# Kernel tuning notes

Hardware: AMD Instinct MI355X
Metric: run time of the kernel (lower is better)

The kernel has to match this reference:

```python
import jax, jax.numpy as jnp
import numpy as np

B, D, S, E = 256, 5, 30, 768
H1, H2, FF, OUT = 512, 512, 256, 2


def setup_inputs() -> dict:
    key = jax.random.key(0)
    ks = iter(jax.random.split(key, 40))

    def p(shape, scale=0.05):
        return jax.random.normal(next(ks), shape, jnp.float32) * scale

    return {
        "sentence_feats": jax.random.normal(next(ks), (B, D, S, E), jnp.float32),
        "time_feats": jax.random.uniform(next(ks), (B, D, S), jnp.float32),
        "len_tweets": jax.random.randint(next(ks), (B, D), 1, S + 1, jnp.int32),
        # TimeLSTM (lstm1)
        "Wd_w": p((H1, H1)), "Wd_b": p((H1,)),
        "Wall_w": p((4 * H1, H1)), "Wall_b": p((4 * H1,)),
        "Uall_w": p((4 * H1, E)), "Uall_b": p((4 * H1,)),
        # attn1
        "A1_W1_w": p((H1, H1)), "A1_W1_b": p((H1,)),
        "A1_W2_w": p((H1, H1)), "A1_W2_b": p((H1,)),
        "A1_V_w": p((1, H1)), "A1_V_b": p((1,)),
        # nn.LSTM (lstm2), gate order i,f,g,o
        "L2_Wih": p((4 * H2, H1)), "L2_Whh": p((4 * H2, H2)),
        "L2_bih": p((4 * H2,)), "L2_bhh": p((4 * H2,)),
        # attn2
        "A2_W1_w": p((H2, H2)), "A2_W1_b": p((H2,)),
        "A2_W2_w": p((H2, H2)), "A2_W2_b": p((H2,)),
        "A2_V_w": p((1, H2)), "A2_V_b": p((1,)),
        # head
        "lin3_w": p((FF, H2)), "lin3_b": p((FF,)),
        "lin4_w": p((OUT, FF)), "lin4_b": p((OUT,)),
    }


def _time_lstm(x, t, Wd_w, Wd_b, Wall_w, Wall_b, Uall_w, Uall_b):
    # x: (N,S,E), t: (N,S) -> o-gate outputs (N,S,H) (the torch module stacks `o`, not `h`)
    N = x.shape[0]
    H = Wd_w.shape[0]
    ux = jnp.einsum('nse,ge->nsg', x, Uall_w) + Uall_b  # (N,S,4H), hoisted out of recurrence

    def step(carry, inp):
        h, c = carry
        ux_s, t_s = inp
        c_s1 = jnp.tanh(c @ Wd_w.T + Wd_b)
        c_adj = c - c_s1 + c_s1 * t_s[:, None]
        gates = jax.nn.sigmoid(h @ Wall_w.T + Wall_b + ux_s)
        f, i, o, c_tmp = jnp.split(gates, 4, axis=1)  # all sigmoid, incl. c_tmp (as in source)
        c = f * c_adj + i * c_tmp
        h = o * jnp.tanh(c)
        return (h, c), o

    init = (jnp.zeros((N, H), x.dtype), jnp.zeros((N, H), x.dtype))
    _, os = jax.lax.scan(step, init, (ux.transpose(1, 0, 2), t.T))
    return os.transpose(1, 0, 2)  # (N,S,H)


def _std_lstm(x, Wih, Whh, bih, bhh):
    # PyTorch nn.LSTM, 1 layer, batch_first. x: (B,T,I) -> (hs (B,T,H), h_n (B,H))
    Bn = x.shape[0]
    H = Whh.shape[1]
    xi = jnp.einsum('bti,gi->btg', x, Wih) + bih + bhh  # (B,T,4H)

    def step(carry, xi_t):
        h, c = carry
        g = xi_t + h @ Whh.T
        i, f, gg, o = jnp.split(g, 4, axis=1)
        c = jax.nn.sigmoid(f) * c + jax.nn.sigmoid(i) * jnp.tanh(gg)
        h = jax.nn.sigmoid(o) * jnp.tanh(c)
        return (h, c), h

    init = (jnp.zeros((Bn, H), x.dtype), jnp.zeros((Bn, H), x.dtype))
    (h_n, _), hs = jax.lax.scan(step, init, xi.transpose(1, 0, 2))
    return hs.transpose(1, 0, 2), h_n


def _forward(sentence_feats, time_feats, Wd_w, Wd_b, Wall_w, Wall_b, Uall_w, Uall_b,
             A1_W1_w, A1_W1_b, A1_W2_w, A1_W2_b, A1_V_w, A1_V_b,
             L2_Wih, L2_Whh, L2_bih, L2_bhh,
             A2_W1_w, A2_W1_b, A2_W2_w, A2_W2_b, A2_V_w, A2_V_b,
             lin3_w, lin3_b, lin4_w, lin4_b, len_tweets):
    x = sentence_feats.transpose(1, 0, 2, 3)  # (D,B,S,E)
    t = time_feats.transpose(1, 0, 2)         # (D,B,S)
    lens = len_tweets.transpose(1, 0)          # (D,B)
    d, b, s, e = x.shape

    # run TimeLSTM over all days at once (days are independent, shared zero init)
    outs = _time_lstm(x.reshape(d * b, s, e), t.reshape(d * b, s),
                      Wd_w, Wd_b, Wall_w, Wall_b, Uall_w, Uall_b).reshape(d, b, s, H1)

    # Faithful to the source's inner loop: temp_hn ends up as the LAST batch
    # element's output at index len-1, shared across the whole batch of that day.
    idx = lens[:, -1] - 1  # (D,)
    last = jnp.take_along_axis(outs[:, -1], idx[:, None, None], axis=1)[:, 0]  # (D,H1)

    # attn1: score = V(tanh(W1(last) + W2(full))), mask by lens, softmax over S
    s1 = jnp.tanh((last @ A1_W1_w.T + A1_W1_b)[:, None, None, :]
                  + jnp.einsum('dbsh,gh->dbsg', outs, A1_W2_w) + A1_W2_b)
    score = jnp.einsum('dbsh,oh->dbso', s1, A1_V_w) + A1_V_b  # (D,B,S,1)
    mask = jnp.arange(s)[None, None, :] < lens[:, :, None]     # (D,B,S)
    score = jnp.where(mask[..., None], score, -jnp.inf)
    aw = jax.nn.softmax(score, axis=2)
    lstm1_out = jnp.sum(aw * outs, axis=2).transpose(1, 0, 2)  # (B,D,H1)

    lstm2_out, hn2 = _std_lstm(lstm1_out, L2_Wih, L2_Whh, L2_bih, L2_bhh)  # (B,D,H2),(B,H2)

    # attn2 over days
    s2 = jnp.tanh((hn2 @ A2_W1_w.T + A2_W1_b)[:, None, :]
                  + lstm2_out @ A2_W2_w.T + A2_W2_b)
    score2 = s2 @ A2_V_w.T + A2_V_b                 # (B,D,1)
    aw2 = jax.nn.softmax(score2, axis=1)
    ctx = jnp.sum(aw2 * lstm2_out, axis=1)          # (B,H2)

    h3 = jax.nn.relu(ctx @ lin3_w.T + lin3_b)       # dropout = identity (eval mode)
    return h3 @ lin4_w.T + lin4_b                   # (B,OUT)


def reference(sentence_feats, time_feats, len_tweets, Wd_w, Wd_b, Wall_w, Wall_b, Uall_w, Uall_b,
              A1_W1_w, A1_W1_b, A1_W2_w, A1_W2_b, A1_V_w, A1_V_b,
              L2_Wih, L2_Whh, L2_bih, L2_bhh,
              A2_W1_w, A2_W1_b, A2_W2_w, A2_W2_b, A2_V_w, A2_V_b,
              lin3_w, lin3_b, lin4_w, lin4_b):
    return _forward(sentence_feats, time_feats, Wd_w, Wd_b, Wall_w, Wall_b, Uall_w, Uall_b,
                    A1_W1_w, A1_W1_b, A1_W2_w, A1_W2_b, A1_V_w, A1_V_b,
                    L2_Wih, L2_Whh, L2_bih, L2_bhh,
                    A2_W1_w, A2_W1_b, A2_W2_w, A2_W2_b, A2_V_w, A2_V_b,
                    lin3_w, lin3_b, lin4_w, lin4_b, len_tweets)
```

## Files before the change

### kernel.cpp

```cpp
#include <hip/hip_runtime.h>
#include <math.h>

typedef _Float16 f16;
typedef _Float16 f16x4 __attribute__((ext_vector_type(4)));
typedef _Float16 f16x8 __attribute__((ext_vector_type(8)));
typedef float f32x4 __attribute__((ext_vector_type(4)));

#define DEV static __device__ __forceinline__

#define OFF_X16    ((size_t)0)
#define OFF_UX     ((size_t)58982400)
#define OFF_OUTS   ((size_t)216268800)
#define OFF_WD     ((size_t)255590400)
#define OFF_WALLP  ((size_t)256114688)
#define OFF_UP     ((size_t)258211840)
#define OFF_W2     ((size_t)261357568)
#define OFF_WIHP   ((size_t)261881856)
#define OFF_WHHP   ((size_t)263979008)
#define OFF_A2W1C  ((size_t)266076160)
#define OFF_A2W2C  ((size_t)266600448)
#define OFF_L3WC   ((size_t)267124736)
#define OFF_BALLP  ((size_t)267386880)
#define OFF_BIHP   ((size_t)267395072)
#define OFF_H16    ((size_t)267403264)
#define OFF_C16    ((size_t)270024704)
#define OFF_C32    ((size_t)272646144)
#define WS_NEED    ((size_t)277889024)
#define OFF_SCORE  ((size_t)0)
#define OFF_W1L    ((size_t)153600)
#define OFF_L1O32  ((size_t)163840)
#define OFF_L1O16  ((size_t)2785280)
#define OFF_XI2    ((size_t)4096000)
#define OFF_C2     ((size_t)14581760)
#define OFF_H2     ((size_t)15630336)
#define OFF_L2O32  ((size_t)16154624)
#define OFF_L2O16  ((size_t)18776064)
#define OFF_U2     ((size_t)20086784)
#define OFF_V2     ((size_t)22708224)
#define OFF_CTX16  ((size_t)23232512)
#define OFF_H3     ((size_t)23494656)

DEV float sigf(float x) { return 1.f / (1.f + __expf(-x)); }
DEV float tanhfast(float x) { float e = __expf(2.f * x); return 1.f - 2.f / (e + 1.f); }
DEV int permrow(int c) { return (((c >> 4) & 3) << 9) | ((c >> 6) << 4) | (c & 15); }

DEV void gload16(const f16* g, f16x8* lds) {
  __builtin_amdgcn_global_load_lds((const __attribute__((address_space(1))) void*)g,
                                   (__attribute__((address_space(3))) void*)lds, 16, 0, 0);
}

DEV void gemm_core(const f16* __restrict__ A, const f16* __restrict__ Bt, int K,
                   int rowBase, int colBase, f16x8* sh, f32x4 (&acc)[4][4]) {
  const int t = threadIdx.x, lane = t & 63, w = t >> 6;
  const int wr = (w >> 1) * 64, wc = (w & 1) * 64;
  const f16* Arow = A + (size_t)rowBase * K;
  const f16* Brow = Bt + (size_t)colBase * K;
  auto stage = [&](f16x8* dstBase, const f16* src, int k0) {
#pragma unroll
    for (int i = 0; i < 4; ++i) {
      int c = i * 256 + t; int r = c >> 3; int cc = (c & 7) ^ (r & 7);
      gload16(src + (size_t)r * K + (k0 + cc * 8), dstBase + i * 256 + (t & 192));
    }
  };
  stage(sh, Arow, 0);
  stage(sh + 2048, Brow, 0);
  const int nk = K >> 6;
  for (int kt = 0; kt < nk; ++kt) {
    const int cur = kt & 1;
    if (kt + 1 < nk) {
      stage(sh + (cur ^ 1) * 1024, Arow, (kt + 1) * 64);
      stage(sh + 2048 + (cur ^ 1) * 1024, Brow, (kt + 1) * 64);
      asm volatile("s_waitcnt vmcnt(8)" ::: "memory");
    } else {
      asm volatile("s_waitcnt vmcnt(0)" ::: "memory");
    }
    __builtin_amdgcn_s_barrier();
    __builtin_amdgcn_sched_barrier(0);
    const f16x8* shA = sh + cur * 1024;
    const f16x8* shB = sh + 2048 + cur * 1024;
    const int rr = lane & 15, chb = lane >> 4;
#pragma unroll
    for (int kk = 0; kk < 2; ++kk) {
      const int ch = kk * 4 + chb;
      f16x8 af[4], bf[4];
#pragma unroll
      for (int m = 0; m < 4; ++m) { int row = wr + m * 16 + rr; af[m] = shA[row * 8 + (ch ^ (row & 7))]; }
#pragma unroll
      for (int n = 0; n < 4; ++n) { int row = wc + n * 16 + rr; bf[n] = shB[row * 8 + (ch ^ (row & 7))]; }
#pragma unroll
      for (int m = 0; m < 4; ++m)
#pragma unroll
        for (int n = 0; n < 4; ++n)
          acc[m][n] = __builtin_amdgcn_mfma_f32_16x16x32_f16(af[m], bf[n], acc[m][n], 0, 0, 0);
    }
    __builtin_amdgcn_sched_barrier(0);
    __builtin_amdgcn_s_barrier();
  }
}

template <int ACT, bool O32, bool O16>
__global__ __launch_bounds__(256, 2) void k_gemm(const f16* __restrict__ A, const f16* __restrict__ Bt,
                                                 int K, int N, const float* __restrict__ bias,
                                                 float* __restrict__ C32, f16* __restrict__ C16) {
  __shared__ f16x8 sh[4096];
  const int rb = blockIdx.y * 128, cb = blockIdx.x * 128;
  f32x4 acc[4][4] = {};
  gemm_core(A, Bt, K, rb, cb, sh, acc);
  const int t = threadIdx.x, lane = t & 63, w = t >> 6;
  const int wr = (w >> 1) * 64, wc = (w & 1) * 64, ec = lane & 15, er = (lane >> 4) * 4;
#pragma unroll
  for (int m = 0; m < 4; ++m)
#pragma unroll
    for (int n = 0; n < 4; ++n) {
      const int c = cb + wc + n * 16 + ec;
      const float bv = bias ? bias[c] : 0.f;
#pragma unroll
      for (int j = 0; j < 4; ++j) {
        const int r = rb + wr + m * 16 + er + j;
        float v = acc[m][n][j] + bv;
        if (ACT == 3) v = fmaxf(v, 0.f);
        if (O32) C32[(size_t)r * N + c] = v;
        if (O16) C16[(size_t)r * N + c] = (f16)v;
      }
    }
}

__global__ __launch_bounds__(256, 1) void k_stepf(
    const f16* __restrict__ hin, const f16* __restrict__ cin16, const float* __restrict__ cin32,
    const f16* __restrict__ Wallp, const f16* __restrict__ Wd16,
    const f16* __restrict__ ux, const float* __restrict__ ballp, const float* __restrict__ Wd_b,
    const float* __restrict__ tf,
    float* __restrict__ cout32, f16* __restrict__ cout16, f16* __restrict__ hout,
    f16* __restrict__ outs, int s) {
  __shared__ f16x8 shA[2048];
  __shared__ f16x8 shB[2048];
  __shared__ f16x8 shC[2048];
  __shared__ f16x8 shD[512];
  const int t = threadIdx.x, lane = t & 63, w = t >> 6;
  const int rb = (blockIdx.x >> 4) * 128;
  const int cg = blockIdx.x & 15;
  const int wr = (w >> 1) * 64, wc = (w & 1) * 64;
  const int rr = lane & 15, chb = lane >> 4;
  f32x4 acc[4][4] = {};
  f32x4 acc2[4] = {};
  const f16* Ah = hin + (size_t)rb * 512;
  const f16* Bw = Wallp + (size_t)cg * 128 * 512;
  const f16* Ac = cin16 + (size_t)rb * 512;
  const f16* Bd = Wd16 + (size_t)cg * 32 * 512;

  auto stage128 = [&](f16x8* dstBase, const f16* src, int k0) {
#pragma unroll
    for (int i = 0; i < 4; ++i) {
      int c = i * 256 + t; int r = c >> 3; int cc = (c & 7) ^ (r & 7);
      gload16(src + (size_t)r * 512 + (k0 + cc * 8), dstBase + i * 256 + (t & 192));
    }
  };
  auto stage32 = [&](f16x8* dstBase, const f16* src, int k0) {
    const int r = t >> 3; const int cc = (t & 7) ^ (r & 7);
    gload16(src + (size_t)r * 512 + (k0 + cc * 8), dstBase + (t & 192));
  };
  stage128(shA, Ah, 0);
  stage128(shB, Bw, 0);
  stage128(shC, Ac, 0);
  stage32(shD, Bd, 0);

  for (int kt = 0; kt < 8; ++kt) {
    const int cur = kt & 1;
    if (kt < 7) {
      stage128(shA + (cur ^ 1) * 1024, Ah, (kt + 1) * 64);
      stage128(shB + (cur ^ 1) * 1024, Bw, (kt + 1) * 64);
      stage128(shC + (cur ^ 1) * 1024, Ac, (kt + 1) * 64);
      stage32(shD + (cur ^ 1) * 256, Bd, (kt + 1) * 64);
      asm volatile("s_waitcnt vmcnt(13)" ::: "memory");
    } else {
      asm volatile("s_waitcnt vmcnt(0)" ::: "memory");
    }
    __builtin_amdgcn_s_barrier();
    __builtin_amdgcn_sched_barrier(0);
    const f16x8* pA = shA + cur * 1024;
    const f16x8* pB = shB + cur * 1024;
    const f16x8* pC = shC + cur * 1024;
    const f16x8* pD = shD + cur * 256;
#pragma unroll
    for (int kk = 0; kk < 2; ++kk) {
      const int ch = kk * 4 + chb;
      f16x8 af[4], bf[4], cf[4], df;
#pragma unroll
      for (int m = 0; m < 4; ++m) {
        const int row = wr + m * 16 + rr;
        af[m] = pA[row * 8 + (ch ^ (row & 7))];
        cf[m] = pC[row * 8 + (ch ^ (row & 7))];
      }
#pragma unroll
      for (int n = 0; n < 4; ++n) { const int row = wc + n * 16 + rr; bf[n] = pB[row * 8 + (ch ^ (row & 7))]; }
      { const int row = (w & 1) * 16 + rr; df = pD[row * 8 + (ch ^ (row & 7))]; }
#pragma unroll
      for (int m = 0; m < 4; ++m) {
#pragma unroll
        for (int n = 0; n < 4; ++n)
          acc[m][n] = __builtin_amdgcn_mfma_f32_16x16x32_f16(af[m], bf[n], acc[m][n], 0, 0, 0);
        acc2[m] = __builtin_amdgcn_mfma_f32_16x16x32_f16(cf[m], df, acc2[m], 0, 0, 0);
      }
    }
    __builtin_amdgcn_sched_barrier(0);
    __builtin_amdgcn_s_barrier();
  }

  const int ec = lane & 15, er = (lane >> 4) * 4;
  const int h = cg * 32 + (w & 1) * 16 + ec;
  float bW[4];
#pragma unroll
  for (int n = 0; n < 4; ++n) bW[n] = ballp[cg * 128 + wc + n * 16 + ec];
  const float bD = Wd_b[h];
#pragma unroll
  for (int m = 0; m < 4; ++m)
#pragma unroll
    for (int j = 0; j < 4; ++j) {
      const int r = rb + wr + m * 16 + er + j;
      const int d = r >> 8, b = r & 255;
      const float tv = tf[((size_t)b * 5 + d) * 30 + s];
      const size_t uxb = ((size_t)r * 30 + s) * 2048 + cg * 128 + wc + ec;
      const float p0 = acc[m][0][j] + bW[0] + (float)ux[uxb];
      const float p1 = acc[m][1][j] + bW[1] + (float)ux[uxb + 16];
      const float p2 = acc[m][2][j] + bW[2] + (float)ux[uxb + 32];
      const float p3 = acc[m][3][j] + bW[3] + (float)ux[uxb + 48];
      const float f = sigf(p0), i = sigf(p1), o = sigf(p2), ct = sigf(p3);
      const float cs = tanhfast(acc2[m][j] + bD);
      const float c_old = cin32[(size_t)r * 512 + h];
      const float cadj = c_old - cs + cs * tv;
      const float cn = f * cadj + i * ct;
      cout32[(size_t)r * 512 + h] = cn;
      cout16[(size_t)r * 512 + h] = (f16)cn;
      hout[(size_t)r * 512 + h] = (f16)(o * tanhfast(cn));
      outs[((size_t)r * 30 + s) * 512 + h] = (f16)o;
    }
}

__global__ __launch_bounds__(256, 2) void k_l2step(const f16* __restrict__ hin, const f16* __restrict__ Whhp,
    const float* __restrict__ xi2, const float* __restrict__ cin, float* __restrict__ cout,
    f16* __restrict__ hout, float* __restrict__ l2o32, f16* __restrict__ l2o16, int ts) {
  __shared__ f16x8 sh[4096];
  const int rb = (blockIdx.x >> 4) * 128, cg = blockIdx.x & 15;
  f32x4 acc[4][4] = {};
  gemm_core(hin, Whhp, 512, rb, cg * 128, sh, acc);
  const int t = threadIdx.x, lane = t & 63, w = t >> 6;
  const int wr = (w >> 1) * 64, wc = (w & 1) * 64, ec = lane & 15, er = (lane >> 4) * 4;
  const int h = cg * 32 + (w & 1) * 16 + ec;
#pragma unroll
  for (int m = 0; m < 4; ++m)
#pragma unroll
    for (int j = 0; j < 4; ++j) {
      const int r = rb + wr + m * 16 + er + j;
      const size_t xb = ((size_t)r * 5 + ts) * 2048 + cg * 128 + wc + ec;
      const float p0 = acc[m][0][j] + xi2[xb];
      const float p1 = acc[m][1][j] + xi2[xb + 16];
      const float p2 = acc[m][2][j] + xi2[xb + 32];
      const float p3 = acc[m][3][j] + xi2[xb + 48];
      const float ii = sigf(p0), ff = sigf(p1), gg = tanhfast(p2), oo = sigf(p3);
      const float cn = ff * cin[(size_t)r * 512 + h] + ii * gg;
      const float hn = oo * tanhfast(cn);
      cout[(size_t)r * 512 + h] = cn;
      hout[(size_t)r * 512 + h] = (f16)hn;
      const size_t ob = ((size_t)r * 5 + ts) * 512 + h;
      l2o32[ob] = hn;
      l2o16[ob] = (f16)hn;
    }
}

__global__ __launch_bounds__(256, 2) void k_score(const f16* __restrict__ outs, const f16* __restrict__ W2t,
    const float* __restrict__ W2b, const float* __restrict__ w1l, const float* __restrict__ V,
    float* __restrict__ score) {
  __shared__ f16x8 sh[4096];
  const int rb = blockIdx.y * 128, cb = blockIdx.x * 128;
  f32x4 acc[4][4] = {};
  gemm_core(outs, W2t, 512, rb, cb, sh, acc);
  const int t = threadIdx.x, lane = t & 63, w = t >> 6;
  const int wr = (w >> 1) * 64, wc = (w & 1) * 64, ec = lane & 15, er = (lane >> 4) * 4;
  float* sacc = (float*)sh;
  if (t < 128) sacc[t] = 0.f;
  __syncthreads();
#pragma unroll
  for (int m = 0; m < 4; ++m)
#pragma unroll
    for (int j = 0; j < 4; ++j) {
      const int lr = wr + m * 16 + er + j;
      const int r = rb + lr;
      const int d = (r / 30) >> 8;
      float p = 0.f;
#pragma unroll
      for (int n = 0; n < 4; ++n) {
        const int c = cb + wc + n * 16 + ec;
        p += V[c] * tanhfast(acc[m][n][j] + W2b[c] + w1l[d * 512 + c]);
      }
      p += __shfl_xor(p, 1); p += __shfl_xor(p, 2); p += __shfl_xor(p, 4); p += __shfl_xor(p, 8);
      if (ec == 0) atomicAdd(&sacc[lr], p);
    }
  __syncthreads();
  if (t < 128) atomicAdd(&score[rb + t], sacc[t]);
}

__global__ __launch_bounds__(256) void k_w1last(const f16* __restrict__ outs, const int* __restrict__ lens,
                                                const float* __restrict__ W1, const float* __restrict__ W1b,
                                                float* __restrict__ w1l) {
  __shared__ float lastv[512];
  const int d = blockIdx.x;
  const int idx = lens[255 * 5 + d] - 1;
  const size_t row = ((size_t)(d * 256 + 255) * 30 + idx) * 512;
  for (int h = threadIdx.x; h < 512; h += 256) lastv[h] = (float)outs[row + h];
  __syncthreads();
  for (int h = threadIdx.x; h < 512; h += 256) {
    const float* wr = W1 + (size_t)h * 512;
    float p = W1b[h];
    for (int k = 0; k < 512; ++k) p += lastv[k] * wr[k];
    w1l[d * 512 + h] = p;
  }
}

__global__ __launch_bounds__(256) void k_attn1(const float* __restrict__ score, const f16* __restrict__ outs,
                                               const int* __restrict__ lens,
// ... 96 lines not shown
  const float* wr = W4 + o * 256;
  float p = b4[o];
  for (int j = 0; j < 256; ++j) p += hr[j] * wr[j];
  out[idx] = p;
}

__global__ __launch_bounds__(256) void k_castx(const float* __restrict__ sf, f16* __restrict__ x16) {
  const int total = 7372800;
  for (int e = blockIdx.x * 256 + threadIdx.x; e < total; e += gridDim.x * 256) {
    const int row = e / 192, k = e - row * 192;
    const int b = row / 150, rem = row - b * 150;
    const int d = rem / 30, s = rem - d * 30;
    const int orow = (d * 256 + b) * 30 + s;
    const float4 v = ((const float4*)sf)[e];
    f16x4 o = {(f16)v.x, (f16)v.y, (f16)v.z, (f16)v.w};
    ((f16x4*)x16)[(size_t)orow * 192 + k] = o;
  }
}

struct CastArgs { const float* src[5]; f16* dst[5]; int cnt4[5]; };
__global__ __launch_bounds__(256) void k_castw(CastArgs a) {
  int g = blockIdx.x * 256 + threadIdx.x;
#pragma unroll
  for (int si = 0; si < 5; ++si) {
    if (g < a.cnt4[si]) {
      const float4 v = ((const float4*)a.src[si])[g];
      f16x4 o = {(f16)v.x, (f16)v.y, (f16)v.z, (f16)v.w};
      ((f16x4*)a.dst[si])[g] = o;
      return;
    }
    g -= a.cnt4[si];
  }
}

struct PermArgs { const float* src[4]; f16* dst[4]; int k4[4]; int cnt4[4]; };
__global__ __launch_bounds__(256) void k_castperm(PermArgs a) {
  int g = blockIdx.x * 256 + threadIdx.x;
#pragma unroll
  for (int si = 0; si < 4; ++si) {
    if (g < a.cnt4[si]) {
      const int K4 = a.k4[si];
      const int c = g / K4, k = g - c * K4;
      const float4 v = ((const float4*)a.src[si])[(size_t)permrow(c) * K4 + k];
      f16x4 o = {(f16)v.x, (f16)v.y, (f16)v.z, (f16)v.w};
      ((f16x4*)a.dst[si])[(size_t)c * K4 + k] = o;
      return;
    }
    g -= a.cnt4[si];
  }
}

__global__ __launch_bounds__(256) void k_zero(f16* h16a, f16* c16a, float* c32a,
    float* ballp, float* bihp, const float* Wall_b, const float* Uall_b,
    const float* bih, const float* bhh) {
  const int i = blockIdx.x * 256 + threadIdx.x;
  if (i < 655360) { h16a[i] = (f16)0.f; c16a[i] = (f16)0.f; c32a[i] = 0.f; }
  if (i < 2048) {
    const int p = permrow(i);
    ballp[i] = Wall_b[p] + Uall_b[p];
    bihp[i] = bih[p] + bhh[p];
  }
}

__global__ __launch_bounds__(256) void k_scoreinit(float* score, const float* Vb, f16* h2a, float* c2a) {
  const int i = blockIdx.x * 256 + threadIdx.x;
  if (i < 38400) score[i] = Vb[0];
  if (i < 131072) { h2a[i] = (f16)0.f; c2a[i] = 0.f; }
}

extern "C" void kernel_launch(void* const* d_in, const int* in_sizes, int n_in,
                              void* d_out, int out_size, void* d_ws, size_t ws_size,
                              hipStream_t stream) {
  const float* sf     = (const float*)d_in[0];
  const float* tf     = (const float*)d_in[1];
  const int*   lens   = (const int*)d_in[2];
  const float* Wd_w   = (const float*)d_in[3];
  const float* Wd_b   = (const float*)d_in[4];
  const float* Wall_w = (const float*)d_in[5];
  const float* Wall_b = (const float*)d_in[6];
  const float* Uall_w = (const float*)d_in[7];
  const float* Uall_b = (const float*)d_in[8];
  const float* A1W1   = (const float*)d_in[9];
  const float* A1W1b  = (const float*)d_in[10];
  const float* A1W2   = (const float*)d_in[11];
  const float* A1W2b  = (const float*)d_in[12];
  const float* A1V    = (const float*)d_in[13];
  const float* A1Vb   = (const float*)d_in[14];
  const float* Wih    = (const float*)d_in[15];
  const float* Whh    = (const float*)d_in[16];
  const float* bih    = (const float*)d_in[17];
  const float* bhh    = (const float*)d_in[18];
  const float* A2W1   = (const float*)d_in[19];
  const float* A2W1b  = (const float*)d_in[20];
  const float* A2W2   = (const float*)d_in[21];
  const float* A2W2b  = (const float*)d_in[22];
  const float* A2V    = (const float*)d_in[23];
  const float* A2Vb   = (const float*)d_in[24];
  const float* L3w    = (const float*)d_in[25];
  const float* L3b    = (const float*)d_in[26];
  const float* L4w    = (const float*)d_in[27];
  const float* L4b    = (const float*)d_in[28];

  if (ws_size < WS_NEED) return;
  char* ws = (char*)d_ws;
  f16*   x16    = (f16*)(ws + OFF_X16);
  f16*   ux16   = (f16*)(ws + OFF_UX);
  f16*   outs16 = (f16*)(ws + OFF_OUTS);
  f16*   Wd16   = (f16*)(ws + OFF_WD);
  f16*   Wallp  = (f16*)(ws + OFF_WALLP);
  f16*   U16p   = (f16*)(ws + OFF_UP);
  f16*   W216   = (f16*)(ws + OFF_W2);
  f16*   Wihp   = (f16*)(ws + OFF_WIHP);
  f16*   Whhp   = (f16*)(ws + OFF_WHHP);
  f16*   A2W116 = (f16*)(ws + OFF_A2W1C);
  f16*   A2W216 = (f16*)(ws + OFF_A2W2C);
  f16*   L316   = (f16*)(ws + OFF_L3WC);
  float* ballp  = (float*)(ws + OFF_BALLP);
  float* bihp   = (float*)(ws + OFF_BIHP);
  f16*   h16b[2]  = {(f16*)(ws + OFF_H16), (f16*)(ws + OFF_H16 + 1310720)};
  f16*   c16b[2]  = {(f16*)(ws + OFF_C16), (f16*)(ws + OFF_C16 + 1310720)};
  float* c32b[2]  = {(float*)(ws + OFF_C32), (float*)(ws + OFF_C32 + 2621440)};
  float* score  = (float*)(ws + OFF_SCORE);
  float* w1l    = (float*)(ws + OFF_W1L);
  float* l1o32  = (float*)(ws + OFF_L1O32);
  f16*   l1o16  = (f16*)(ws + OFF_L1O16);
  float* xi2    = (float*)(ws + OFF_XI2);
  float* c2b[2] = {(float*)(ws + OFF_C2), (float*)(ws + OFF_C2 + 524288)};
  f16*   h2b[2] = {(f16*)(ws + OFF_H2), (f16*)(ws + OFF_H2 + 262144)};
  float* l2o32  = (float*)(ws + OFF_L2O32);
  f16*   l2o16  = (f16*)(ws + OFF_L2O16);
  float* u2     = (float*)(ws + OFF_U2);
  float* v2     = (float*)(ws + OFF_V2);
  f16*   ctx16  = (f16*)(ws + OFF_CTX16);
  float* h3     = (float*)(ws + OFF_H3);

  k_castx<<<2048, 256, 0, stream>>>(sf, x16);
  CastArgs ca;
  ca.src[0] = Wd_w;  ca.dst[0] = Wd16;   ca.cnt4[0] = 65536;
  ca.src[1] = A1W2;  ca.dst[1] = W216;   ca.cnt4[1] = 65536;
  ca.src[2] = A2W1;  ca.dst[2] = A2W116; ca.cnt4[2] = 65536;
  ca.src[3] = A2W2;  ca.dst[3] = A2W216; ca.cnt4[3] = 65536;
  ca.src[4] = L3w;   ca.dst[4] = L316;   ca.cnt4[4] = 32768;
  k_castw<<<1152, 256, 0, stream>>>(ca);
  PermArgs pa;
  pa.src[0] = Wall_w; pa.dst[0] = Wallp; pa.k4[0] = 128; pa.cnt4[0] = 262144;
  pa.src[1] = Uall_w; pa.dst[1] = U16p;  pa.k4[1] = 192; pa.cnt4[1] = 393216;
  pa.src[2] = Wih;    pa.dst[2] = Wihp;  pa.k4[2] = 128; pa.cnt4[2] = 262144;
  pa.src[3] = Whh;    pa.dst[3] = Whhp;  pa.k4[3] = 128; pa.cnt4[3] = 262144;
  k_castperm<<<4608, 256, 0, stream>>>(pa);
  k_zero<<<2560, 256, 0, stream>>>(h16b[0], c16b[0], c32b[0], ballp, bihp, Wall_b, Uall_b, bih, bhh);

  k_gemm<0, false, true><<<dim3(16, 300), 256, 0, stream>>>(x16, U16p, 768, 2048, nullptr, nullptr, ux16);

  for (int s = 0; s < 30; ++s) {
    const int pi = s & 1, po = pi ^ 1;
    k_stepf<<<160, 256, 0, stream>>>(h16b[pi], c16b[pi], c32b[pi], Wallp, Wd16, ux16, ballp, Wd_b, tf,
                                     c32b[po], c16b[po], h16b[po], outs16, s);
  }

  k_w1last<<<5, 256, 0, stream>>>(outs16, lens, A1W1, A1W1b, w1l);
  k_scoreinit<<<512, 256, 0, stream>>>(score, A1Vb, h2b[0], c2b[0]);
  k_score<<<dim3(4, 300), 256, 0, stream>>>(outs16, W216, A1W2b, w1l, A1V, score);
  k_attn1<<<1280, 256, 0, stream>>>(score, outs16, lens, l1o32, l1o16);

  k_gemm<0, true, false><<<dim3(16, 10), 256, 0, stream>>>(l1o16, Wihp, 512, 2048, bihp, xi2, nullptr);
  for (int ts = 0; ts < 5; ++ts) {
    const int pi = ts & 1, po = pi ^ 1;
    k_l2step<<<32, 256, 0, stream>>>(h2b[pi], Whhp, xi2, c2b[pi], c2b[po], h2b[po], l2o32, l2o16, ts);
  }

  k_uv<<<48, 256, 0, stream>>>(l2o16, A2W216, h2b[1], A2W116, A2W2b, A2W1b, u2, v2);
  k_attn2<<<256, 256, 0, stream>>>(u2, v2, l2o32, A2V, A2Vb, ctx16);

  k_gemm<3, true, false><<<dim3(2, 2), 256, 0, stream>>>(ctx16, L316, 512, 256, L3b, h3, nullptr);
  k_final<<<2, 256, 0, stream>>>(h3, L4w, L4b, (float*)d_out);
}
```

Before: 1.090 ms.

## Fuse LSTM time-step loops into persistent kernels with grid barriers

Replaces the 30 per-step TimeLSTM launches and the 5 per-step LSTM2 launches with one persistent kernel each, synchronised between steps by an atomic-counter grid barrier. The per-step ux slice and fp32 cell state are now prefetched into LDS with swizzled async loads that overlap the GEMM, and time features are pre-transposed so the loads are coalesced. Step 0 skips the GEMM because the initial state is zero. This removes launch overhead and uncoalesced epilogue loads. It relies on all 160 blocks being co-resident for the spin barrier, which risks deadlock if they are not.

```diff
diff --git a/kernel.cpp b/kernel.cpp
--- a/kernel.cpp
+++ b/kernel.cpp
@@ -39,6 +39,8 @@
 #define OFF_V2     ((size_t)22708224)
 #define OFF_CTX16  ((size_t)23232512)
 #define OFF_H3     ((size_t)23494656)
+#define OFF_TFT    ((size_t)23756800)
+#define OFF_CNT    ((size_t)23910400)
 
 DEV float sigf(float x) { return 1.f / (1.f + __expf(-x)); }
 DEV float tanhfast(float x) { float e = __expf(2.f * x); return 1.f - 2.f / (e + 1.f); }
@@ -47,6 +49,18 @@
 DEV void gload16(const f16* g, f16x8* lds) {
   __builtin_amdgcn_global_load_lds((const __attribute__((address_space(1))) void*)g,
                                    (__attribute__((address_space(3))) void*)lds, 16, 0, 0);
+}
+
+DEV void grid_barrier(unsigned* cnt, unsigned target) {
+  __syncthreads();
+  if (threadIdx.x == 0) {
+    __threadfence();
+    __hip_atomic_fetch_add(cnt, 1u, __ATOMIC_RELEASE, __HIP_MEMORY_SCOPE_AGENT);
+    while (__hip_atomic_load(cnt, __ATOMIC_ACQUIRE, __HIP_MEMORY_SCOPE_AGENT) < target)
+      __builtin_amdgcn_s_sleep(1);
+  }
+  __syncthreads();
+  __threadfence();
 }
 
 DEV void gemm_core(const f16* __restrict__ A, const f16* __restrict__ Bt, int K,
@@ -125,28 +139,37 @@
     }
 }
 
-__global__ __launch_bounds__(256, 1) void k_stepf(
-    const f16* __restrict__ hin, const f16* __restrict__ cin16, const float* __restrict__ cin32,
+__global__ __launch_bounds__(256, 1) void k_steps(
+    f16* __restrict__ h0, f16* __restrict__ h1,
+    f16* __restrict__ c0, f16* __restrict__ c1,
+    float* __restrict__ e0, float* __restrict__ e1,
     const f16* __restrict__ Wallp, const f16* __restrict__ Wd16,
-    const f16* __restrict__ ux, const float* __restrict__ ballp, const float* __restrict__ Wd_b,
-    const float* __restrict__ tf,
-    float* __restrict__ cout32, f16* __restrict__ cout16, f16* __restrict__ hout,
-    f16* __restrict__ outs, int s) {
+    const f16* __restrict__ ux, const float* __restrict__ ballp,
+    const float* __restrict__ Wd_b, const float* __restrict__ tft,
+    f16* __restrict__ outs, unsigned* __restrict__ cnt) {
   __shared__ f16x8 shA[2048];
   __shared__ f16x8 shB[2048];
   __shared__ f16x8 shC[2048];
   __shared__ f16x8 shD[512];
-  const int t = threadIdx.x, lane = t & 63, w = t >> 6;
-  const int rb = (blockIdx.x >> 4) * 128;
-  const int cg = blockIdx.x & 15;
+  __shared__ f16x8 shU[2048];
+  __shared__ f16x8 shE[1024];
+  const int t = threadIdx.x, lane = t & 63, w = t >> 6;
+  const int rb = ((int)blockIdx.x >> 4) * 128;
+  const int cg = (int)blockIdx.x & 15;
   const int wr = (w >> 1) * 64, wc = (w & 1) * 64;
   const int rr = lane & 15, chb = lane >> 4;
-  f32x4 acc[4][4] = {};
-  f32x4 acc2[4] = {};
-  const f16* Ah = hin + (size_t)rb * 512;
+  const int ec = lane & 15, er = (lane >> 4) * 4;
+  const int h = cg * 32 + (w & 1) * 16 + ec;
+  const int hcol = (w & 1) * 16 + ec;
   const f16* Bw = Wallp + (size_t)cg * 128 * 512;
-  const f16* Ac = cin16 + (size_t)rb * 512;
   const f16* Bd = Wd16 + (size_t)cg * 32 * 512;
+  float bW[4];
+#pragma unroll
+  for (int n = 0; n < 4; ++n) bW[n] = ballp[cg * 128 + wc + n * 16 + ec];
+  const float bD = Wd_b[h];
+  const f16* shUf = (const f16*)shU;
+  const float* shEf = (const float*)shE;
+  const int kbase = (wc >> 3) + (ec >> 3);
 
   auto stage128 = [&](f16x8* dstBase, const f16* src, int k0) {
 #pragma unroll
@@ -159,112 +182,162 @@
     const int r = t >> 3; const int cc = (t & 7) ^ (r & 7);
     gload16(src + (size_t)r * 512 + (k0 + cc * 8), dstBase + (t & 192));
   };
-  stage128(shA, Ah, 0);
-  stage128(shB, Bw, 0);
-  stage128(shC, Ac, 0);
-  stage32(shD, Bd, 0);
-
-  for (int kt = 0; kt < 8; ++kt) {
-    const int cur = kt & 1;
-    if (kt < 7) {
-      stage128(shA + (cur ^ 1) * 1024, Ah, (kt + 1) * 64);
-      stage128(shB + (cur ^ 1) * 1024, Bw, (kt + 1) * 64);
-      stage128(shC + (cur ^ 1) * 1024, Ac, (kt + 1) * 64);
-      stage32(shD + (cur ^ 1) * 256, Bd, (kt + 1) * 64);
-      asm volatile("s_waitcnt vmcnt(13)" ::: "memory");
+  auto stageU = [&](int s) {
+#pragma unroll
+    for (int i = 0; i < 8; ++i) {
+      int c = i * 256 + t; int lr = c >> 4; int k = c & 15;
+      int klog = k ^ (((lr >> 2) & 3) << 1);
+      gload16(ux + ((size_t)(rb + lr) * 30 + s) * 2048 + cg * 128 + klog * 8,
+              shU + i * 256 + (t & 192));
+    }
+  };
+  auto stageE = [&](const float* ein) {
+#pragma unroll
+    for (int i = 0; i < 4; ++i) {
+      int c = i * 256 + t; int lr = c >> 3; int k = c & 7;
+      int klog = k ^ (((lr >> 2) & 1) << 2);
+      gload16((const f16*)(ein + (size_t)(rb + lr) * 512 + cg * 32 + klog * 4),
+              shE + i * 256 + (t & 192));
+    }
+  };
+
+  for (int s = 0; s < 30; ++s) {
+    const f16* hin = (s & 1) ? h1 : h0;
+    const f16* cin = (s & 1) ? c1 : c0;
+    const float* ein = (s & 1) ? e1 : e0;
+    f16* hout = (s & 1) ? h0 : h1;
+    f16* cout16 = (s & 1) ? c0 : c1;
+    float* eout = (s & 1) ? e0 : e1;
+    const f16* Ah = hin + (size_t)rb * 512;
+    const f16* Ac = cin + (size_t)rb * 512;
+    f32x4 acc[4][4] = {};
+    f32x4 acc2[4] = {};
+
+    if (s == 0) {
+      stageU(s);
+      stageE(ein);
+      asm volatile("s_waitcnt vmcnt(0)" ::: "memory");
+      __builtin_amdgcn_s_barrier();
     } else {
-      asm volatile("s_waitcnt vmcnt(0)" ::: "memory");
-    }
-    __builtin_amdgcn_s_barrier();
-    __builtin_amdgcn_sched_barrier(0);
-    const f16x8* pA = shA + cur * 1024;
-    const f16x8* pB = shB + cur * 1024;
-    const f16x8* pC = shC + cur * 1024;
-    const f16x8* pD = shD + cur * 256;
-#pragma unroll
-    for (int kk = 0; kk < 2; ++kk) {
-      const int ch = kk * 4 + chb;
-      f16x8 af[4], bf[4], cf[4], df;
-#pragma unroll
-      for (int m = 0; m < 4; ++m) {
-        const int row = wr + m * 16 + rr;
-        af[m] = pA[row * 8 + (ch ^ (row & 7))];
-        cf[m] = pC[row * 8 + (ch ^ (row & 7))];
+      stage128(shA, Ah, 0);
+      stage128(shB, Bw, 0);
+      stage128(shC, Ac, 0);
+      stage32(shD, Bd, 0);
+      stageU(s);
+      stageE(ein);
+      for (int kt = 0; kt < 8; ++kt) {
+        const int cur = kt & 1;
+        if (kt < 7) {
+          stage128(shA + (cur ^ 1) * 1024, Ah, (kt + 1) * 64);
+          stage128(shB + (cur ^ 1) * 1024, Bw, (kt + 1) * 64);
+          stage128(shC + (cur ^ 1) * 1024, Ac, (kt + 1) * 64);
+          stage32(shD + (cur ^ 1) * 256, Bd, (kt + 1) * 64);
+          asm volatile("s_waitcnt vmcnt(13)" ::: "memory");
+        } else {
+          asm volatile("s_waitcnt vmcnt(0)" ::: "memory");
+        }
+        __builtin_amdgcn_s_barrier();
+        __builtin_amdgcn_sched_barrier(0);
+        const f16x8* pA = shA + cur * 1024;
+        const f16x8* pB = shB + cur * 1024;
+        const f16x8* pC = shC + cur * 1024;
+        const f16x8* pD = shD + cur * 256;
+#pragma unroll
+        for (int kk = 0; kk < 2; ++kk) {
+          const int ch = kk * 4 + chb;
+          f16x8 af[4], bf[4], cf[4], df;
+#pragma unroll
+          for (int m = 0; m < 4; ++m) {
+            const int row = wr + m * 16 + rr;
+            af[m] = pA[row * 8 + (ch ^ (row & 7))];
+            cf[m] = pC[row * 8 + (ch ^ (row & 7))];
+          }
+#pragma unroll
+          for (int n = 0; n < 4; ++n) { const int row = wc + n * 16 + rr; bf[n] = pB[row * 8 + (ch ^ (row & 7))]; }
+          { const int row = (w & 1) * 16 + rr; df = pD[row * 8 + (ch ^ (row & 7))]; }
+#pragma unroll
+          for (int m = 0; m < 4; ++m) {
+#pragma unroll
+            for (int n = 0; n < 4; ++n)
+              acc[m][n] = __builtin_amdgcn_mfma_f32_16x16x32_f16(af[m], bf[n], acc[m][n], 0, 0, 0);
+            acc2[m] = __builtin_amdgcn_mfma_f32_16x16x32_f16(cf[m], df, acc2[m], 0, 0, 0);
+          }
+        }
+        __builtin_amdgcn_sched_barrier(0);
+        __builtin_amdgcn_s_barrier();
       }
-#pragma unroll
-      for (int n = 0; n < 4; ++n) { const int row = wc + n * 16 + rr; bf[n] = pB[row * 8 + (ch ^ (row & 7))]; }
-      { const int row = (w & 1) * 16 + rr; df = pD[row * 8 + (ch ^ (row & 7))]; }
-#pragma unroll
-      for (int m = 0; m < 4; ++m) {
-#pragma unroll
-        for (int n = 0; n < 4; ++n)
-          acc[m][n] = __builtin_amdgcn_mfma_f32_16x16x32_f16(af[m], bf[n], acc[m][n], 0, 0, 0);
-        acc2[m] = __builtin_amdgcn_mfma_f32_16x16x32_f16(cf[m], df, acc2[m], 0, 0, 0);
+    }
+
+#pragma unroll
+    for (int m = 0; m < 4; ++m)
+#pragma unroll
+      for (int j = 0; j < 4; ++j) {
+        const int lr = wr + m * 16 + er + j;
+        const int r = rb + lr;
+        const float tv = tft[s * 1280 + r];
+        const int sU = ((lr >> 2) & 3) << 1;
+        const float u0 = (float)shUf[(lr * 16 + ((kbase + 0) ^ sU)) * 8 + (ec & 7)];
+        const float u1 = (float)shUf[(lr * 16 + ((kbase + 2) ^ sU)) * 8 + (ec & 7)];
+        const float u2v = (float)shUf[(lr * 16 + ((kbase + 4) ^ sU)) * 8 + (ec & 7)];
+        const float u3 = (float)shUf[(lr * 16 + ((kbase + 6) ^ sU)) * 8 + (ec & 7)];
+        const float p0 = acc[m][0][j] + bW[0] + u0;
+        const float p1 = acc[m][1][j] + bW[1] + u1;
+        const float p2 = acc[m][2][j] + bW[2] + u2v;
+        const float p3 = acc[m][3][j] + bW[3] + u3;
+        const float f = sigf(p0), i = sigf(p1), o = sigf(p2), ct = sigf(p3);
+        const float cs = tanhfast(acc2[m][j] + bD);
+        const int sE = ((lr >> 2) & 1) << 2;
+        const float c_old = shEf[(lr * 8 + ((hcol >> 2) ^ sE)) * 4 + (hcol & 3)];
+        const float cadj = c_old - cs + cs * tv;
+        const float cn = f * cadj + i * ct;
+        eout[(size_t)r * 512 + h] = cn;
+        cout16[(size_t)r * 512 + h] = (f16)cn;
+        hout[(size_t)r * 512 + h] = (f16)(o * tanhfast(cn));
+        outs[((size_t)r * 30 + s) * 512 + h] = (f16)o;
       }
-    }
-    __builtin_amdgcn_sched_barrier(0);
-    __builtin_amdgcn_s_barrier();
-  }
-
-  const int ec = lane & 15, er = (lane >> 4) * 4;
-  const int h = cg * 32 + (w & 1) * 16 + ec;
-  float bW[4];
-#pragma unroll
-  for (int n = 0; n < 4; ++n) bW[n] = ballp[cg * 128 + wc + n * 16 + ec];
-  const float bD = Wd_b[h];
-#pragma unroll
-  for (int m = 0; m < 4; ++m)
-#pragma unroll
-    for (int j = 0; j < 4; ++j) {
-      const int r = rb + wr + m * 16 + er + j;
-      const int d = r >> 8, b = r & 255;
-      const float tv = tf[((size_t)b * 5 + d) * 30 + s];
-      const size_t uxb = ((size_t)r * 30 + s) * 2048 + cg * 128 + wc + ec;
-      const float p0 = acc[m][0][j] + bW[0] + (float)ux[uxb];
-      const float p1 = acc[m][1][j] + bW[1] + (float)ux[uxb + 16];
-      const float p2 = acc[m][2][j] + bW[2] + (float)ux[uxb + 32];
-      const float p3 = acc[m][3][j] + bW[3] + (float)ux[uxb + 48];
-      const float f = sigf(p0), i = sigf(p1), o = sigf(p2), ct = sigf(p3);
-      const float cs = tanhfast(acc2[m][j] + bD);
-      const float c_old = cin32[(size_t)r * 512 + h];
-      const float cadj = c_old - cs + cs * tv;
-      const float cn = f * cadj + i * ct;
-      cout32[(size_t)r * 512 + h] = cn;
-      cout16[(size_t)r * 512 + h] = (f16)cn;
-      hout[(size_t)r * 512 + h] = (f16)(o * tanhfast(cn));
-      outs[((size_t)r * 30 + s) * 512 + h] = (f16)o;
-    }
-}
-
-__global__ __launch_bounds__(256, 2) void k_l2step(const f16* __restrict__ hin, const f16* __restrict__ Whhp,
-    const float* __restrict__ xi2, const float* __restrict__ cin, float* __restrict__ cout,
-    f16* __restrict__ hout, float* __restrict__ l2o32, f16* __restrict__ l2o16, int ts) {
+
+    if (s < 29) grid_barrier(cnt, 160u * (unsigned)(s + 1));
+  }
+}
+
+__global__ __launch_bounds__(256, 2) void k_l2steps(
+    f16* __restrict__ h20, f16* __restrict__ h21,
+    float* __restrict__ c20, float* __restrict__ c21,
+    const f16* __restrict__ Whhp, const float* __restrict__ xi2,
+    float* __restrict__ l2o32, f16* __restrict__ l2o16, unsigned* __restrict__ cnt) {
   __shared__ f16x8 sh[4096];
-  const int rb = (blockIdx.x >> 4) * 128, cg = blockIdx.x & 15;
-  f32x4 acc[4][4] = {};
-  gemm_core(hin, Whhp, 512, rb, cg * 128, sh, acc);
+  const int rb = ((int)blockIdx.x >> 4) * 128, cg = (int)blockIdx.x & 15;
   const int t = threadIdx.x, lane = t & 63, w = t >> 6;
   const int wr = (w >> 1) * 64, wc = (w & 1) * 64, ec = lane & 15, er = (lane >> 4) * 4;
   const int h = cg * 32 + (w & 1) * 16 + ec;
-#pragma unroll
-  for (int m = 0; m < 4; ++m)
-#pragma unroll
-    for (int j = 0; j < 4; ++j) {
-      const int r = rb + wr + m * 16 + er + j;
-      const size_t xb = ((size_t)r * 5 + ts) * 2048 + cg * 128 + wc + ec;
-      const float p0 = acc[m][0][j] + xi2[xb];
-      const float p1 = acc[m][1][j] + xi2[xb + 16];
-      const float p2 = acc[m][2][j] + xi2[xb + 32];
-      const float p3 = acc[m][3][j] + xi2[xb + 48];
-      const float ii = sigf(p0), ff = sigf(p1), gg = tanhfast(p2), oo = sigf(p3);
-      const float cn = ff * cin[(size_t)r * 512 + h] + ii * gg;
-      const float hn = oo * tanhfast(cn);
-      cout[(size_t)r * 512 + h] = cn;
-      hout[(size_t)r * 512 + h] = (f16)hn;
-      const size_t ob = ((size_t)r * 5 + ts) * 512 + h;
-      l2o32[ob] = hn;
-      l2o16[ob] = (f16)hn;
-    }
+  for (int ts = 0; ts < 5; ++ts) {
+    const f16* hin = (ts & 1) ? h21 : h20;
+    const float* cin = (ts & 1) ? c21 : c20;
+    f16* hout = (ts & 1) ? h20 : h21;
+    float* cout = (ts & 1) ? c20 : c21;
+    f32x4 acc[4][4] = {};
+    if (ts > 0) gemm_core(hin, Whhp, 512, rb, cg * 128, sh, acc);
+#pragma unroll
+    for (int m = 0; m < 4; ++m)
+#pragma unroll
+      for (int j = 0; j < 4; ++j) {
+        const int r = rb + wr + m * 16 + er + j;
+        const size_t xb = ((size_t)r * 5 + ts) * 2048 + cg * 128 + wc + ec;
+        const float p0 = acc[m][0][j] + xi2[xb];
+        const float p1 = acc[m][1][j] + xi2[xb + 16];
+        const float p2 = acc[m][2][j] + xi2[xb + 32];
+        const float p3 = acc[m][3][j] + xi2[xb + 48];
+        const float ii = sigf(p0), ff = sigf(p1), gg = tanhfast(p2), oo = sigf(p3);
+        const float cn = ff * cin[(size_t)r * 512 + h] + ii * gg;
+        const float hn = oo * tanhfast(cn);
+        cout[(size_t)r * 512 + h] = cn;
+        hout[(size_t)r * 512 + h] = (f16)hn;
+        const size_t ob = ((size_t)r * 5 + ts) * 512 + h;
+        l2o32[ob] = hn;
+        l2o16[ob] = (f16)hn;
+      }
+    if (ts < 4) grid_barrier(cnt, 32u * (unsigned)(ts + 1));
+  }
 }
 
 __global__ __launch_bounds__(256, 2) void k_score(const f16* __restrict__ outs, const f16* __restrict__ W2t,
@@ -467,7 +540,7 @@
 
 __global__ __launch_bounds__(256) void k_zero(f16* h16a, f16* c16a, float* c32a,
     float* ballp, float* bihp, const float* Wall_b, const float* Uall_b,
-    const float* bih, const float* bhh) {
+    const float* bih, const float* bhh, float* tft, const float* tf, unsigned* cnt) {
   const int i = blockIdx.x * 256 + threadIdx.x;
   if (i < 655360) { h16a[i] = (f16)0.f; c16a[i] = (f16)0.f; c32a[i] = 0.f; }
   if (i < 2048) {
@@ -475,6 +548,12 @@
     ballp[i] = Wall_b[p] + Uall_b[p];
     bihp[i] = bih[p] + bhh[p];
   }
+  if (i < 38400) {
+    const int s = i / 1280, r = i - s * 1280;
+    const int d = r >> 8, b = r & 255;
+    tft[i] = tf[((size_t)b * 5 + d) * 30 + s];
+  }
+  if (i < 2) cnt[i] = 0u;
 }
 
 __global__ __launch_bounds__(256) void k_scoreinit(float* score, const float* Vb, f16* h2a, float* c2a) {
@@ -548,6 +627,8 @@
   float* v2     = (float*)(ws + OFF_V2);
   f16*   ctx16  = (f16*)(ws + OFF_CTX16);
   float* h3     = (float*)(ws + OFF_H3);
+  float* tft    = (float*)(ws + OFF_TFT);
+  unsigned* cnt = (unsigned*)(ws + OFF_CNT);
 
   k_castx<<<2048, 256, 0, stream>>>(sf, x16);
   CastArgs ca;
@@ -563,15 +644,14 @@
   pa.src[2] = Wih;    pa.dst[2] = Wihp;  pa.k4[2] = 128; pa.cnt4[2] = 262144;
   pa.src[3] = Whh;    pa.dst[3] = Whhp;  pa.k4[3] = 128; pa.cnt4[3] = 262144;
   k_castperm<<<4608, 256, 0, stream>>>(pa);
-  k_zero<<<2560, 256, 0, stream>>>(h16b[0], c16b[0], c32b[0], ballp, bihp, Wall_b, Uall_b, bih, bhh);
 
   k_gemm<0, false, true><<<dim3(16, 300), 256, 0, stream>>>(x16, U16p, 768, 2048, nullptr, nullptr, ux16);
 
-  for (int s = 0; s < 30; ++s) {
-    const int pi = s & 1, po = pi ^ 1;
-    k_stepf<<<160, 256, 0, stream>>>(h16b[pi], c16b[pi], c32b[pi], Wallp, Wd16, ux16, ballp, Wd_b, tf,
-                                     c32b[po], c16b[po], h16b[po], outs16, s);
-  }
+  k_zero<<<2560, 256, 0, stream>>>(h16b[0], c16b[0], c32b[0], ballp, bihp, Wall_b, Uall_b, bih, bhh,
+                                   tft, tf, cnt);
+
+  k_steps<<<160, 256, 0, stream>>>(h16b[0], h16b[1], c16b[0], c16b[1], c32b[0], c32b[1],
+                                   Wallp, Wd16, ux16, ballp, Wd_b, tft, outs16, cnt);
 
   k_w1last<<<5, 256, 0, stream>>>(outs16, lens, A1W1, A1W1b, w1l);
   k_scoreinit<<<512, 256, 0, stream>>>(score, A1Vb, h2b[0], c2b[0]);
@@ -579,10 +659,7 @@
   k_attn1<<<1280, 256, 0, stream>>>(score, outs16, lens, l1o32, l1o16);
 
   k_gemm<0, true, false><<<dim3(16, 10), 256, 0, stream>>>(l1o16, Wihp, 512, 2048, bihp, xi2, nullptr);
-  for (int ts = 0; ts < 5; ++ts) {
-    const int pi = ts & 1, po = pi ^ 1;
-    k_l2step<<<32, 256, 0, stream>>>(h2b[pi], Whhp, xi2, c2b[pi], c2b[po], h2b[po], l2o32, l2o16, ts);
-  }
+  k_l2steps<<<32, 256, 0, stream>>>(h2b[0], h2b[1], c2b[0], c2b[1], Whhp, xi2, l2o32, l2o16, cnt + 1);
 
   k_uv<<<48, 256, 0, stream>>>(l2o16, A2W216, h2b[1], A2W116, A2W2b, A2W1b, u2, v2);
   k_attn2<<<256, 256, 0, stream>>>(u2, v2, l2o32, A2V, A2Vb, ctx16);
```

New measurement: 1.584 ms. +45.4%, slower.

## Prefetch ux and cell state into LDS during step GEMM, skip first-step GEMM

Applied to the files above, without the earlier changes.

The time-LSTM step kernel now loads its ux gate slice and fp32 cell-state tile into swizzled shared memory with asynchronous global-to-LDS loads. These loads are issued alongside the GEMM pipeline, so the epilogue reads shared memory instead of doing scattered global reads after the matmul. At step 0 the recurrent GEMM is skipped because h and c start at zero. Time features are pre-transposed into a per-step contiguous buffer inside the zero-init kernel, which now runs after the ux GEMM because the new buffer shares workspace with the x16 region. The cost is about 49KB more LDS per block and more outstanding loads during the main loop.

```diff
diff --git a/kernel.cpp b/kernel.cpp
--- a/kernel.cpp
+++ b/kernel.cpp
@@ -39,6 +39,7 @@
 #define OFF_V2     ((size_t)22708224)
 #define OFF_CTX16  ((size_t)23232512)
 #define OFF_H3     ((size_t)23494656)
+#define OFF_TFT    ((size_t)23756800)
 
 DEV float sigf(float x) { return 1.f / (1.f + __expf(-x)); }
 DEV float tanhfast(float x) { float e = __expf(2.f * x); return 1.f - 2.f / (e + 1.f); }
@@ -129,24 +130,36 @@
     const f16* __restrict__ hin, const f16* __restrict__ cin16, const float* __restrict__ cin32,
     const f16* __restrict__ Wallp, const f16* __restrict__ Wd16,
     const f16* __restrict__ ux, const float* __restrict__ ballp, const float* __restrict__ Wd_b,
-    const float* __restrict__ tf,
+    const float* __restrict__ tft,
     float* __restrict__ cout32, f16* __restrict__ cout16, f16* __restrict__ hout,
     f16* __restrict__ outs, int s) {
   __shared__ f16x8 shA[2048];
   __shared__ f16x8 shB[2048];
   __shared__ f16x8 shC[2048];
   __shared__ f16x8 shD[512];
-  const int t = threadIdx.x, lane = t & 63, w = t >> 6;
-  const int rb = (blockIdx.x >> 4) * 128;
-  const int cg = blockIdx.x & 15;
+  __shared__ f16x8 shU[2048];
+  __shared__ f16x8 shE[1024];
+  const int t = threadIdx.x, lane = t & 63, w = t >> 6;
+  const int rb = ((int)blockIdx.x >> 4) * 128;
+  const int cg = (int)blockIdx.x & 15;
   const int wr = (w >> 1) * 64, wc = (w & 1) * 64;
   const int rr = lane & 15, chb = lane >> 4;
+  const int ec = lane & 15, er = (lane >> 4) * 4;
+  const int h = cg * 32 + (w & 1) * 16 + ec;
+  const int hcol = (w & 1) * 16 + ec;
+  const f16* Ah = hin + (size_t)rb * 512;
+  const f16* Ac = cin16 + (size_t)rb * 512;
+  const f16* Bw = Wallp + (size_t)cg * 128 * 512;
+  const f16* Bd = Wd16 + (size_t)cg * 32 * 512;
+  float bW[4];
+#pragma unroll
+  for (int n = 0; n < 4; ++n) bW[n] = ballp[cg * 128 + wc + n * 16 + ec];
+  const float bD = Wd_b[h];
+  const f16* shUf = (const f16*)shU;
+  const float* shEf = (const float*)shE;
+  const int kbase = (wc >> 3) + (ec >> 3);
   f32x4 acc[4][4] = {};
   f32x4 acc2[4] = {};
-  const f16* Ah = hin + (size_t)rb * 512;
-  const f16* Bw = Wallp + (size_t)cg * 128 * 512;
-  const f16* Ac = cin16 + (size_t)rb * 512;
-  const f16* Bd = Wd16 + (size_t)cg * 32 * 512;
 
   auto stage128 = [&](f16x8* dstBase, const f16* src, int k0) {
 #pragma unroll
@@ -159,74 +172,100 @@
     const int r = t >> 3; const int cc = (t & 7) ^ (r & 7);
     gload16(src + (size_t)r * 512 + (k0 + cc * 8), dstBase + (t & 192));
   };
-  stage128(shA, Ah, 0);
-  stage128(shB, Bw, 0);
-  stage128(shC, Ac, 0);
-  stage32(shD, Bd, 0);
-
-  for (int kt = 0; kt < 8; ++kt) {
-    const int cur = kt & 1;
-    if (kt < 7) {
-      stage128(shA + (cur ^ 1) * 1024, Ah, (kt + 1) * 64);
-      stage128(shB + (cur ^ 1) * 1024, Bw, (kt + 1) * 64);
-      stage128(shC + (cur ^ 1) * 1024, Ac, (kt + 1) * 64);
-      stage32(shD + (cur ^ 1) * 256, Bd, (kt + 1) * 64);
-      asm volatile("s_waitcnt vmcnt(13)" ::: "memory");
-    } else {
-      asm volatile("s_waitcnt vmcnt(0)" ::: "memory");
-    }
+  auto stageU = [&]() {
+#pragma unroll
+    for (int i = 0; i < 8; ++i) {
+      int c = i * 256 + t; int lr = c >> 4; int k = c & 15;
+      int klog = k ^ (((lr >> 2) & 3) << 1);
+      gload16(ux + ((size_t)(rb + lr) * 30 + s) * 2048 + cg * 128 + klog * 8,
+              shU + i * 256 + (t & 192));
+    }
+  };
+  auto stageE = [&]() {
+#pragma unroll
+    for (int i = 0; i < 4; ++i) {
+      int c = i * 256 + t; int lr = c >> 3; int k = c & 7;
+      int klog = k ^ (((lr >> 2) & 1) << 2);
+      gload16((const f16*)(cin32 + (size_t)(rb + lr) * 512 + cg * 32 + klog * 4),
+              shE + i * 256 + (t & 192));
+    }
+  };
+
+  if (s == 0) {
+    stageU();
+    stageE();
+    asm volatile("s_waitcnt vmcnt(0)" ::: "memory");
     __builtin_amdgcn_s_barrier();
-    __builtin_amdgcn_sched_barrier(0);
-    const f16x8* pA = shA + cur * 1024;
-    const f16x8* pB = shB + cur * 1024;
-    const f16x8* pC = shC + cur * 1024;
-    const f16x8* pD = shD + cur * 256;
-#pragma unroll
-    for (int kk = 0; kk < 2; ++kk) {
-      const int ch = kk * 4 + chb;
-      f16x8 af[4], bf[4], cf[4], df;
-#pragma unroll
-      for (int m = 0; m < 4; ++m) {
-        const int row = wr + m * 16 + rr;
-        af[m] = pA[row * 8 + (ch ^ (row & 7))];
-        cf[m] = pC[row * 8 + (ch ^ (row & 7))];
+  } else {
+    stage128(shA, Ah, 0);
+    stage128(shB, Bw, 0);
+    stage128(shC, Ac, 0);
+    stage32(shD, Bd, 0);
+    stageU();
+    stageE();
+    for (int kt = 0; kt < 8; ++kt) {
+      const int cur = kt & 1;
+      if (kt < 7) {
+        stage128(shA + (cur ^ 1) * 1024, Ah, (kt + 1) * 64);
+        stage128(shB + (cur ^ 1) * 1024, Bw, (kt + 1) * 64);
+        stage128(shC + (cur ^ 1) * 1024, Ac, (kt + 1) * 64);
+        stage32(shD + (cur ^ 1) * 256, Bd, (kt + 1) * 64);
+        asm volatile("s_waitcnt vmcnt(13)" ::: "memory");
+      } else {
+        asm volatile("s_waitcnt vmcnt(0)" ::: "memory");
       }
-#pragma unroll
-      for (int n = 0; n < 4; ++n) { const int row = wc + n * 16 + rr; bf[n] = pB[row * 8 + (ch ^ (row & 7))]; }
-      { const int row = (w & 1) * 16 + rr; df = pD[row * 8 + (ch ^ (row & 7))]; }
-#pragma unroll
-      for (int m = 0; m < 4; ++m) {
-#pragma unroll
-        for (int n = 0; n < 4; ++n)
-          acc[m][n] = __builtin_amdgcn_mfma_f32_16x16x32_f16(af[m], bf[n], acc[m][n], 0, 0, 0);
-        acc2[m] = __builtin_amdgcn_mfma_f32_16x16x32_f16(cf[m], df, acc2[m], 0, 0, 0);
+      __builtin_amdgcn_s_barrier();
+      __builtin_amdgcn_sched_barrier(0);
+      const f16x8* pA = shA + cur * 1024;
+      const f16x8* pB = shB + cur * 1024;
+      const f16x8* pC = shC + cur * 1024;
+      const f16x8* pD = shD + cur * 256;
+#pragma unroll
+      for (int kk = 0; kk < 2; ++kk) {
+        const int ch = kk * 4 + chb;
+        f16x8 af[4], bf[4], cf[4], df;
+#pragma unroll
+        for (int m = 0; m < 4; ++m) {
+          const int row = wr + m * 16 + rr;
+          af[m] = pA[row * 8 + (ch ^ (row & 7))];
+          cf[m] = pC[row * 8 + (ch ^ (row & 7))];
+        }
+#pragma unroll
+        for (int n = 0; n < 4; ++n) { const int row = wc + n * 16 + rr; bf[n] = pB[row * 8 + (ch ^ (row & 7))]; }
+        { const int row = (w & 1) * 16 + rr; df = pD[row * 8 + (ch ^ (row & 7))]; }
+#pragma unroll
+        for (int m = 0; m < 4; ++m) {
+#pragma unroll
+          for (int n = 0; n < 4; ++n)
+            acc[m][n] = __builtin_amdgcn_mfma_f32_16x16x32_f16(af[m], bf[n], acc[m][n], 0, 0, 0);
+          acc2[m] = __builtin_amdgcn_mfma_f32_16x16x32_f16(cf[m], df, acc2[m], 0, 0, 0);
+        }
       }
-    }
-    __builtin_amdgcn_sched_barrier(0);
-    __builtin_amdgcn_s_barrier();
-  }
-
-  const int ec = lane & 15, er = (lane >> 4) * 4;
-  const int h = cg * 32 + (w & 1) * 16 + ec;
-  float bW[4];
-#pragma unroll
-  for (int n = 0; n < 4; ++n) bW[n] = ballp[cg * 128 + wc + n * 16 + ec];
-  const float bD = Wd_b[h];
+      __builtin_amdgcn_sched_barrier(0);
+      __builtin_amdgcn_s_barrier();
+    }
+  }
+
 #pragma unroll
   for (int m = 0; m < 4; ++m)
 #pragma unroll
     for (int j = 0; j < 4; ++j) {
-      const int r = rb + wr + m * 16 + er + j;
-      const int d = r >> 8, b = r & 255;
-      const float tv = tf[((size_t)b * 5 + d) * 30 + s];
-      const size_t uxb = ((size_t)r * 30 + s) * 2048 + cg * 128 + wc + ec;
-      const float p0 = acc[m][0][j] + bW[0] + (float)ux[uxb];
-      const float p1 = acc[m][1][j] + bW[1] + (float)ux[uxb + 16];
-      const float p2 = acc[m][2][j] + bW[2] + (float)ux[uxb + 32];
-      const float p3 = acc[m][3][j] + bW[3] + (float)ux[uxb + 48];
+      const int lr = wr + m * 16 + er + j;
+      const int r = rb + lr;
+      const float tv = tft[s * 1280 + r];
+      const int sU = ((lr >> 2) & 3) << 1;
+      const float u0 = (float)shUf[(lr * 16 + ((kbase + 0) ^ sU)) * 8 + (ec & 7)];
+      const float u1 = (float)shUf[(lr * 16 + ((kbase + 2) ^ sU)) * 8 + (ec & 7)];
+      const float u2v = (float)shUf[(lr * 16 + ((kbase + 4) ^ sU)) * 8 + (ec & 7)];
+      const float u3 = (float)shUf[(lr * 16 + ((kbase + 6) ^ sU)) * 8 + (ec & 7)];
+      const float p0 = acc[m][0][j] + bW[0] + u0;
+      const float p1 = acc[m][1][j] + bW[1] + u1;
+      const float p2 = acc[m][2][j] + bW[2] + u2v;
+      const float p3 = acc[m][3][j] + bW[3] + u3;
       const float f = sigf(p0), i = sigf(p1), o = sigf(p2), ct = sigf(p3);
       const float cs = tanhfast(acc2[m][j] + bD);
-      const float c_old = cin32[(size_t)r * 512 + h];
+      const int sE = ((lr >> 2) & 1) << 2;
+      const float c_old = shEf[(lr * 8 + ((hcol >> 2) ^ sE)) * 4 + (hcol & 3)];
       const float cadj = c_old - cs + cs * tv;
       const float cn = f * cadj + i * ct;
       cout32[(size_t)r * 512 + h] = cn;
@@ -467,13 +506,18 @@
 
 __global__ __launch_bounds__(256) void k_zero(f16* h16a, f16* c16a, float* c32a,
     float* ballp, float* bihp, const float* Wall_b, const float* Uall_b,
-    const float* bih, const float* bhh) {
+    const float* bih, const float* bhh, float* tft, const float* tf) {
   const int i = blockIdx.x * 256 + threadIdx.x;
   if (i < 655360) { h16a[i] = (f16)0.f; c16a[i] = (f16)0.f; c32a[i] = 0.f; }
   if (i < 2048) {
     const int p = permrow(i);
     ballp[i] = Wall_b[p] + Uall_b[p];
     bihp[i] = bih[p] + bhh[p];
+  }
+  if (i < 38400) {
+    const int s = i / 1280, r = i - s * 1280;
+    const int d = r >> 8, b = r & 255;
+    tft[i] = tf[((size_t)b * 5 + d) * 30 + s];
   }
 }
 
@@ -548,6 +592,7 @@
   float* v2     = (float*)(ws + OFF_V2);
   f16*   ctx16  = (f16*)(ws + OFF_CTX16);
   float* h3     = (float*)(ws + OFF_H3);
+  float* tft    = (float*)(ws + OFF_TFT);
 
   k_castx<<<2048, 256, 0, stream>>>(sf, x16);
   CastArgs ca;
@@ -563,13 +608,15 @@
   pa.src[2] = Wih;    pa.dst[2] = Wihp;  pa.k4[2] = 128; pa.cnt4[2] = 262144;
   pa.src[3] = Whh;    pa.dst[3] = Whhp;  pa.k4[3] = 128; pa.cnt4[3] = 262144;
   k_castperm<<<4608, 256, 0, stream>>>(pa);
-  k_zero<<<2560, 256, 0, stream>>>(h16b[0], c16b[0], c32b[0], ballp, bihp, Wall_b, Uall_b, bih, bhh);
 
   k_gemm<0, false, true><<<dim3(16, 300), 256, 0, stream>>>(x16, U16p, 768, 2048, nullptr, nullptr, ux16);
+
+  k_zero<<<2560, 256, 0, stream>>>(h16b[0], c16b[0], c32b[0], ballp, bihp, Wall_b, Uall_b, bih, bhh,
+                                   tft, tf);
 
   for (int s = 0; s < 30; ++s) {
     const int pi = s & 1, po = pi ^ 1;
-    k_stepf<<<160, 256, 0, stream>>>(h16b[pi], c16b[pi], c32b[pi], Wallp, Wd16, ux16, ballp, Wd_b, tf,
+    k_stepf<<<160, 256, 0, stream>>>(h16b[pi], c16b[pi], c32b[pi], Wallp, Wd16, ux16, ballp, Wd_b, tft,
                                      c32b[po], c16b[po], h16b[po], outs16, s);
   }
 
```

New measurement: 1.003 ms. 1.09x faster.
